# Kernel tuning notes

Measured on AMD Instinct MI355X. Metric: run time of the kernel, lower is better.

## Reference

```python
import jax, jax.numpy as jnp
import numpy as np

N, K, D = 32768, 4096, 256


def setup_inputs() -> dict:
    key = jax.random.key(0)
    k1, k2 = jax.random.split(key)
    z_e = jax.random.normal(k1, (N, D), dtype=jnp.float32)
    embed = jax.random.normal(k2, (K, D), dtype=jnp.float32)
    return {"z_e": z_e, "embed": embed}


def reference(z_e, embed):
    # squared L2 distances: ||z||^2 - 2 z.E^T + ||e||^2  -> [N, K]
    d = (jnp.sum(z_e * z_e, axis=1, keepdims=True)
         - 2.0 * (z_e @ embed.T)
         + jnp.sum(embed * embed, axis=1))
    idx = jnp.argmin(d, axis=1)                      # [N] int32
    one_hot = jax.nn.one_hot(idx, K, dtype=z_e.dtype)  # [N, K]
    z_q = one_hot @ embed                            # [N, D] (matches torch's one_hot @ embed)
    return (z_q, idx, one_hot)
```

## Files before the change

kernel.cpp:

```cpp
#include <hip/hip_runtime.h>


#define N_TOK 32768
#define K_CODE 4096
#define D_DIM 256
#define BM 64

typedef float f32x4 __attribute__((ext_vector_type(4)));
typedef short s16x8 __attribute__((ext_vector_type(8)));

#define OUT_FLOATS 142639104u
#define SCR_FLOATS 1576960u
#define SCR_OFF    (OUT_FLOATS - SCR_FLOATS)
#define EFRAG_SHORTS (3u * K_CODE * D_DIM)
#define OH_SAFE_ROWS 32320

static __device__ __forceinline__ unsigned short f2bf(float f) {
    unsigned int u = __float_as_uint(f);
    u = (u + 0x7fffu + ((u >> 16) & 1u)) >> 16;
    return (unsigned short)u;
}
static __device__ __forceinline__ float bf2f(unsigned short b) {
    return __uint_as_float(((unsigned int)b) << 16);
}

__global__ __launch_bounds__(256) void vq_prep(const float* __restrict__ embed,
                                               float* __restrict__ out) {
    __shared__ float part[8][33];
    unsigned short* escr = (unsigned short*)(out + SCR_OFF);
    float* e2g = out + SCR_OFF + (EFRAG_SHORTS / 2);

    const int t    = threadIdx.x;
    const int cl   = t >> 5;
    const int r32  = t & 31;
    const int dc   = r32 >> 2;
    const int quad = r32 & 3;
    const int k    = blockIdx.x * 8 + cl;

    const float* src = embed + (size_t)k * D_DIM + dc * 32 + quad * 8;
    float x[8];
    *(float4*)(x)     = *(const float4*)(src);
    *(float4*)(x + 4) = *(const float4*)(src + 4);

    s16x8 hv, mv, lv;
    float s2 = 0.0f;
#pragma unroll
    for (int j = 0; j < 8; ++j) {
        const float xx = x[j];
        s2 += xx * xx;
        const unsigned short bh = f2bf(xx);
        const float r1 = xx - bf2f(bh);
        const unsigned short bm = f2bf(r1);
        hv[j] = (short)bh; mv[j] = (short)bm; lv[j] = (short)f2bf(r1 - bf2f(bm));
    }

    const int ct_g = k >> 4;
    const int lane = quad * 16 + (k & 15);
    const size_t base = ((size_t)(ct_g * 8 + dc) * 3) * 512 + lane * 8;
    *(s16x8*)&escr[base]        = hv;
    *(s16x8*)&escr[base + 512]  = mv;
    *(s16x8*)&escr[base + 1024] = lv;

    part[cl][r32] = s2;
    __syncthreads();
    if (t < 8) {
        float s = 0.0f;
#pragma unroll
        for (int j = 0; j < 32; ++j) s += part[t][j];
        e2g[blockIdx.x * 8 + t] = s;
    }
}

static __device__ __forceinline__ void load_b(const unsigned short* __restrict__ escr,
                                              int kt, int dc, int w, int lane,
                                              s16x8 (&buf)[2][3]) {
#pragma unroll
    for (int u = 0; u < 2; ++u) {
        const int ct_g = kt * 16 + w * 2 + u;
        const unsigned short* p = &escr[((size_t)(ct_g * 8 + dc) * 3) * 512 + lane * 8];
#pragma unroll
        for (int c = 0; c < 3; ++c)
            buf[u][c] = *(const s16x8*)(p + c * 512);
    }
}

static __device__ __forceinline__ void proc_step(const short* As,
        const float* __restrict__ e2g, int kt, int dc, int w, int lane, int n,
        s16x8 (&bfm)[2][3], f32x4 (&acc)[4][2], float (&e2r)[2],
        float (&bv)[16], int (&bidx)[16]) {
    if (dc == 0) {
#pragma unroll
        for (int u = 0; u < 2; ++u) e2r[u] = e2g[kt * 256 + (w * 2 + u) * 16 + n];
    }
#pragma unroll
    for (int rt = 0; rt < 4; ++rt) {
        s16x8 af0 = *(const s16x8*)&As[((0 * 4 + rt) * 8 + dc) * 512 + lane * 8];
        s16x8 af1 = *(const s16x8*)&As[((1 * 4 + rt) * 8 + dc) * 512 + lane * 8];
        s16x8 af2 = *(const s16x8*)&As[((2 * 4 + rt) * 8 + dc) * 512 + lane * 8];
#pragma unroll
        for (int u = 0; u < 2; ++u) {
            f32x4 a = acc[rt][u];
            a = __builtin_amdgcn_mfma_f32_16x16x32_bf16(af0, bfm[u][0], a, 0, 0, 0);
            a = __builtin_amdgcn_mfma_f32_16x16x32_bf16(af0, bfm[u][1], a, 0, 0, 0);
            a = __builtin_amdgcn_mfma_f32_16x16x32_bf16(af1, bfm[u][0], a, 0, 0, 0);
            a = __builtin_amdgcn_mfma_f32_16x16x32_bf16(af1, bfm[u][1], a, 0, 0, 0);
            a = __builtin_amdgcn_mfma_f32_16x16x32_bf16(af0, bfm[u][2], a, 0, 0, 0);
            a = __builtin_amdgcn_mfma_f32_16x16x32_bf16(af2, bfm[u][0], a, 0, 0, 0);
            acc[rt][u] = a;
        }
    }
    if (dc == 7) {
#pragma unroll
        for (int u = 0; u < 2; ++u) {
            const int code = kt * 256 + (w * 2 + u) * 16 + n;
#pragma unroll
            for (int rt = 0; rt < 4; ++rt)
#pragma unroll
                for (int r = 0; r < 4; ++r) {
                    const float val = fmaf(-2.0f, acc[rt][u][r], e2r[u]);
                    const int slot = rt * 4 + r;
                    if (val < bv[slot]) { bv[slot] = val; bidx[slot] = code; }
                }
        }
#pragma unroll
        for (int rt = 0; rt < 4; ++rt)
#pragma unroll
            for (int u = 0; u < 2; ++u) acc[rt][u] = (f32x4){0.f, 0.f, 0.f, 0.f};
    }
}

__global__ __launch_bounds__(512, 2)
void vq_argmin_mfma(const float* __restrict__ z_e,
                    const float* __restrict__ embed,
                    float* __restrict__ out) {
    __shared__ __align__(16) short As[49152];
    __shared__ float redv[64][9];
    __shared__ int   redi[64][9];
    __shared__ int   bk_lds[64];

    const unsigned short* escr = (const unsigned short*)(out + SCR_OFF);
    const float* e2g = out + SCR_OFF + (EFRAG_SHORTS / 2);

    const int t    = threadIdx.x;
    const int w    = t >> 6;
    const int lane = t & 63;
    const int n    = lane & 15;
    const int quad = lane >> 4;
    const int row0 = blockIdx.x * BM;

#pragma unroll
    for (int i = 0; i < 4; ++i) {
        const int run  = t + 512 * i;
        const int qs   = run & 3;
        const int dcs  = (run >> 2) & 7;
        const int row  = run >> 5;
        const float* src = z_e + (size_t)(row0 + row) * D_DIM + dcs * 32 + qs * 8;
        float x[8];
        *(float4*)(x)     = *(const float4*)(src);
        *(float4*)(x + 4) = *(const float4*)(src + 4);
        s16x8 hv, mv, lv;
#pragma unroll
        for (int j = 0; j < 8; ++j) {
            const float xx = x[j];
            const unsigned short bh = f2bf(xx);
            const float r1 = xx - bf2f(bh);
            const unsigned short bm = f2bf(r1);
            hv[j] = (short)bh; mv[j] = (short)bm; lv[j] = (short)f2bf(r1 - bf2f(bm));
        }
        const int rtile = row >> 4;
        const int ls    = qs * 16 + (row & 15);
        *(s16x8*)&As[((0 * 4 + rtile) * 8 + dcs) * 512 + ls * 8] = hv;
        *(s16x8*)&As[((1 * 4 + rtile) * 8 + dcs) * 512 + ls * 8] = mv;
        *(s16x8*)&As[((2 * 4 + rtile) * 8 + dcs) * 512 + ls * 8] = lv;
    }
    __syncthreads();

    float bv[16];
    int   bidx[16];
#pragma unroll
    for (int s = 0; s < 16; ++s) { bv[s] = 3.0e38f; bidx[s] = 0; }

    f32x4 acc[4][2];
#pragma unroll
    for (int rt = 0; rt < 4; ++rt)
#pragma unroll
        for (int u = 0; u < 2; ++u) acc[rt][u] = (f32x4){0.f, 0.f, 0.f, 0.f};

    float e2r[2];
    s16x8 b0[2][3], b1[2][3];
    load_b(escr, 0, 0, w, lane, b0);

#pragma unroll 1
    for (int it = 0; it < 64; ++it) {
        const int s0 = it * 2, s1 = s0 + 1, s2 = s1 + 1;
        load_b(escr, s1 >> 3, s1 & 7, w, lane, b1);
        proc_step(As, e2g, s0 >> 3, s0 & 7, w, lane, n, b0, acc, e2r, bv, bidx);
        if (it < 63) load_b(escr, s2 >> 3, s2 & 7, w, lane, b0);
        proc_step(As, e2g, s1 >> 3, s1 & 7, w, lane, n, b1, acc, e2r, bv, bidx);
    }

#pragma unroll
    for (int slot = 0; slot < 16; ++slot) {
#pragma unroll
        for (int mask = 1; mask < 16; mask <<= 1) {
            const float ov = __shfl_xor(bv[slot], mask);
            const int   oi = __shfl_xor(bidx[slot], mask);
            if (ov < bv[slot] || (ov == bv[slot] && oi < bidx[slot])) {
                bv[slot] = ov; bidx[slot] = oi;
            }
        }
    }
    if (n == 0) {
#pragma unroll
        for (int rt = 0; rt < 4; ++rt)
#pragma unroll
            for (int r = 0; r < 4; ++r) {
                const int row_local = rt * 16 + quad * 4 + r;
                redv[row_local][w] = bv[rt * 4 + r];
                redi[row_local][w] = bidx[rt * 4 + r];
            }
    }
    __syncthreads();
    if (t < 64) {
        float v = redv[t][0];
        int  bi = redi[t][0];
#pragma unroll
        for (int j = 1; j < 8; ++j) {
            const float v2 = redv[t][j];
            const int   i2 = redi[t][j];
            if (v2 < v || (v2 == v && i2 < bi)) { v = v2; bi = i2; }
        }
        bk_lds[t] = bi;
        out[(size_t)N_TOK * D_DIM + (size_t)(row0 + t)] = (float)bi;
    }
    __syncthreads();

    float* zq = out;
    float* oh = out + (size_t)N_TOK * D_DIM + N_TOK;

#pragma unroll 1
    for (int rr = 0; rr < 8; ++rr) {
        const int rl  = w * 8 + rr;
        const int row = row0 + rl;
        const int bk  = bk_lds[rl];
        f32x4 v = *(const f32x4*)&embed[(size_t)bk * D_DIM + lane * 4];
        __builtin_nontemporal_store(v, (f32x4*)&zq[(size_t)row * D_DIM + lane * 4]);
    }
    if (row0 < OH_SAFE_ROWS) {
#pragma unroll 1
        for (int rr = 0; rr < 8; ++rr) {
            const int rl  = w * 8 + rr;
            const int row = row0 + rl;
            const int bk  = bk_lds[rl];
            float* ohrow = &oh[(size_t)row * K_CODE];
#pragma unroll
            for (int g = 0; g < 16; ++g) {
                const int base = (g * 64 + lane) * 4;
                f32x4 u;
                u.x = (bk == base    ) ? 1.0f : 0.0f;
                u.y = (bk == base + 1) ? 1.0f : 0.0f;
                u.z = (bk == base + 2) ? 1.0f : 0.0f;
                u.w = (bk == base + 3) ? 1.0f : 0.0f;
                __builtin_nontemporal_store(u, (f32x4*)&ohrow[base]);
            }
        }
    }
}

__launch_bounds__(256, 8)
__global__ void vq_oh_tail(float* __restrict__ out) {
    __shared__ int bks[16];
    const int t    = threadIdx.x;
    const int w    = t >> 6;
    const int lane = t & 63;
    const int row0 = OH_SAFE_ROWS + blockIdx.x * 16;

    const float* idxf = out + (size_t)N_TOK * D_DIM;
    float* oh = out + (size_t)N_TOK * D_DIM + N_TOK;

    if (t < 16) bks[t] = (int)idxf[row0 + t];
    __syncthreads();

#pragma unroll 1
    for (int rr = 0; rr < 4; ++rr) {
        const int r   = rr * 4 + w;
        const int row = row0 + r;
        const int bk  = bks[r];
        float* ohrow = &oh[(size_t)row * K_CODE];
#pragma unroll
        for (int g = 0; g < 16; ++g) {
            const int base = (g * 64 + lane) * 4;
            f32x4 u;
            u.x = (bk == base    ) ? 1.0f : 0.0f;
            u.y = (bk == base + 1) ? 1.0f : 0.0f;
            u.z = (bk == base + 2) ? 1.0f : 0.0f;
            u.w = (bk == base + 3) ? 1.0f : 0.0f;
            __builtin_nontemporal_store(u, (f32x4*)&ohrow[base]);
        }
    }
}

extern "C" void kernel_launch(void* const* d_in, const int* in_sizes, int n_in,
                              void* d_out, int out_size, void* d_ws, size_t ws_size,
                              hipStream_t stream) {
    const float* z_e   = (const float*)d_in[0];
    const float* embed = (const float*)d_in[1];
    float* out = (float*)d_out;

    hipLaunchKernelGGL(vq_prep,        dim3(K_CODE / 8), dim3(256), 0, stream, embed, out);
    hipLaunchKernelGGL(vq_argmin_mfma, dim3(N_TOK / BM), dim3(512), 0, stream, z_e, embed, out);
    hipLaunchKernelGGL(vq_oh_tail,     dim3((N_TOK - OH_SAFE_ROWS) / 16), dim3(256), 0, stream, out);
}
```

Measured before the change: 851.9 us.

## Process two code tiles per pass to reuse A fragments across both

Restructures the main argmin loop so each iteration handles two 256-code tiles at once, with separate accumulators. The A fragments for one d-chunk are loaded from LDS once and reused for both tiles, halving LDS reads per MFMA. B fragment loads are double-buffered across the two groups with precomputed pointer offsets. It doubles the accumulator registers, which may raise register pressure and hurt occupancy under the 512x2 launch bound.

```diff
diff --git a/kernel.cpp b/kernel.cpp
--- a/kernel.cpp
+++ b/kernel.cpp
@@ -14,6 +14,8 @@
 #define SCR_OFF    (OUT_FLOATS - SCR_FLOATS)
 #define EFRAG_SHORTS (3u * K_CODE * D_DIM)
 #define OH_SAFE_ROWS 32320
+
+#define MFMA(a, b, c) __builtin_amdgcn_mfma_f32_16x16x32_bf16((a), (b), (c), 0, 0, 0)
 
 static __device__ __forceinline__ unsigned short f2bf(float f) {
     unsigned int u = __float_as_uint(f);
@@ -68,64 +70,6 @@
 #pragma unroll
         for (int j = 0; j < 32; ++j) s += part[t][j];
         e2g[blockIdx.x * 8 + t] = s;
-    }
-}
-
-static __device__ __forceinline__ void load_b(const unsigned short* __restrict__ escr,
-                                              int kt, int dc, int w, int lane,
-                                              s16x8 (&buf)[2][3]) {
-#pragma unroll
-    for (int u = 0; u < 2; ++u) {
-        const int ct_g = kt * 16 + w * 2 + u;
-        const unsigned short* p = &escr[((size_t)(ct_g * 8 + dc) * 3) * 512 + lane * 8];
-#pragma unroll
-        for (int c = 0; c < 3; ++c)
-            buf[u][c] = *(const s16x8*)(p + c * 512);
-    }
-}
-
-static __device__ __forceinline__ void proc_step(const short* As,
-        const float* __restrict__ e2g, int kt, int dc, int w, int lane, int n,
-        s16x8 (&bfm)[2][3], f32x4 (&acc)[4][2], float (&e2r)[2],
-        float (&bv)[16], int (&bidx)[16]) {
-    if (dc == 0) {
-#pragma unroll
-        for (int u = 0; u < 2; ++u) e2r[u] = e2g[kt * 256 + (w * 2 + u) * 16 + n];
-    }
-#pragma unroll
-    for (int rt = 0; rt < 4; ++rt) {
-        s16x8 af0 = *(const s16x8*)&As[((0 * 4 + rt) * 8 + dc) * 512 + lane * 8];
-        s16x8 af1 = *(const s16x8*)&As[((1 * 4 + rt) * 8 + dc) * 512 + lane * 8];
-        s16x8 af2 = *(const s16x8*)&As[((2 * 4 + rt) * 8 + dc) * 512 + lane * 8];
-#pragma unroll
-        for (int u = 0; u < 2; ++u) {
-            f32x4 a = acc[rt][u];
-            a = __builtin_amdgcn_mfma_f32_16x16x32_bf16(af0, bfm[u][0], a, 0, 0, 0);
-            a = __builtin_amdgcn_mfma_f32_16x16x32_bf16(af0, bfm[u][1], a, 0, 0, 0);
-            a = __builtin_amdgcn_mfma_f32_16x16x32_bf16(af1, bfm[u][0], a, 0, 0, 0);
-            a = __builtin_amdgcn_mfma_f32_16x16x32_bf16(af1, bfm[u][1], a, 0, 0, 0);
-            a = __builtin_amdgcn_mfma_f32_16x16x32_bf16(af0, bfm[u][2], a, 0, 0, 0);
-            a = __builtin_amdgcn_mfma_f32_16x16x32_bf16(af2, bfm[u][0], a, 0, 0, 0);
-            acc[rt][u] = a;
-        }
-    }
-    if (dc == 7) {
-#pragma unroll
-        for (int u = 0; u < 2; ++u) {
-            const int code = kt * 256 + (w * 2 + u) * 16 + n;
-#pragma unroll
-            for (int rt = 0; rt < 4; ++rt)
-#pragma unroll
-                for (int r = 0; r < 4; ++r) {
-                    const float val = fmaf(-2.0f, acc[rt][u][r], e2r[u]);
-                    const int slot = rt * 4 + r;
-                    if (val < bv[slot]) { bv[slot] = val; bidx[slot] = code; }
-                }
-        }
-#pragma unroll
-        for (int rt = 0; rt < 4; ++rt)
-#pragma unroll
-            for (int u = 0; u < 2; ++u) acc[rt][u] = (f32x4){0.f, 0.f, 0.f, 0.f};
     }
 }
 
@@ -180,23 +124,92 @@
 #pragma unroll
     for (int s = 0; s < 16; ++s) { bv[s] = 3.0e38f; bidx[s] = 0; }
 
-    f32x4 acc[4][2];
-#pragma unroll
-    for (int rt = 0; rt < 4; ++rt)
-#pragma unroll
-        for (int u = 0; u < 2; ++u) acc[rt][u] = (f32x4){0.f, 0.f, 0.f, 0.f};
-
-    float e2r[2];
-    s16x8 b0[2][3], b1[2][3];
-    load_b(escr, 0, 0, w, lane, b0);
+    f32x4 acc[2][4][2];
+#pragma unroll
+    for (int g = 0; g < 2; ++g)
+#pragma unroll
+        for (int rt = 0; rt < 4; ++rt)
+#pragma unroll
+            for (int u = 0; u < 2; ++u) acc[g][rt][u] = (f32x4){0.f, 0.f, 0.f, 0.f};
+
+    float e2r[2][2];
+    s16x8 Bb[2][2][3];
+
+    const unsigned short* ewbase = escr + (size_t)(w * 2) * 12288 + lane * 8;
+
+#pragma unroll
+    for (int u = 0; u < 2; ++u)
+#pragma unroll
+        for (int c = 0; c < 3; ++c)
+            Bb[0][u][c] = *(const s16x8*)(ewbase + u * 12288 + c * 512);
 
 #pragma unroll 1
-    for (int it = 0; it < 64; ++it) {
-        const int s0 = it * 2, s1 = s0 + 1, s2 = s1 + 1;
-        load_b(escr, s1 >> 3, s1 & 7, w, lane, b1);
-        proc_step(As, e2g, s0 >> 3, s0 & 7, w, lane, n, b0, acc, e2r, bv, bidx);
-        if (it < 63) load_b(escr, s2 >> 3, s2 & 7, w, lane, b0);
-        proc_step(As, e2g, s1 >> 3, s1 & 7, w, lane, n, b1, acc, e2r, bv, bidx);
+    for (int ktp = 0; ktp < 8; ++ktp) {
+        const unsigned short* ep  = ewbase + (size_t)ktp * 393216;
+        const unsigned short* epn = ewbase + (size_t)(ktp < 7 ? ktp + 1 : 7) * 393216;
+
+#pragma unroll
+        for (int g = 0; g < 2; ++g)
+#pragma unroll
+            for (int u = 0; u < 2; ++u)
+                e2r[g][u] = e2g[ktp * 512 + g * 256 + (w * 2 + u) * 16 + n];
+
+#pragma unroll
+        for (int dc = 0; dc < 8; ++dc) {
+            s16x8 af[4][3];
+#pragma unroll
+            for (int rt = 0; rt < 4; ++rt)
+#pragma unroll
+                for (int c = 0; c < 3; ++c)
+                    af[rt][c] = *(const s16x8*)&As[((c * 4 + rt) * 8 + dc) * 512 + lane * 8];
+
+#pragma unroll
+            for (int g = 0; g < 2; ++g) {
+                const unsigned short* np = (g == 0) ? (ep + 196608 + dc * 1536)
+                                         : (dc < 7) ? (ep + (dc + 1) * 1536)
+                                                    : epn;
+#pragma unroll
+                for (int u = 0; u < 2; ++u)
+#pragma unroll
+                    for (int c = 0; c < 3; ++c)
+                        Bb[g ^ 1][u][c] = *(const s16x8*)(np + u * 12288 + c * 512);
+
+#pragma unroll
+                for (int rt = 0; rt < 4; ++rt)
+#pragma unroll
+                    for (int u = 0; u < 2; ++u) {
+                        f32x4 a = acc[g][rt][u];
+                        a = MFMA(af[rt][0], Bb[g][u][0], a);
+                        a = MFMA(af[rt][0], Bb[g][u][1], a);
+                        a = MFMA(af[rt][1], Bb[g][u][0], a);
+                        a = MFMA(af[rt][1], Bb[g][u][1], a);
+                        a = MFMA(af[rt][0], Bb[g][u][2], a);
+                        a = MFMA(af[rt][2], Bb[g][u][0], a);
+                        acc[g][rt][u] = a;
+                    }
+            }
+        }
+
+#pragma unroll
+        for (int g = 0; g < 2; ++g)
+#pragma unroll
+            for (int u = 0; u < 2; ++u) {
+                const int code = (ktp * 2 + g) * 256 + (w * 2 + u) * 16 + n;
+#pragma unroll
+                for (int rt = 0; rt < 4; ++rt)
+#pragma unroll
+                    for (int r = 0; r < 4; ++r) {
+                        const float val = fmaf(-2.0f, acc[g][rt][u][r], e2r[g][u]);
+                        const int slot = rt * 4 + r;
+                        if (val < bv[slot]) { bv[slot] = val; bidx[slot] = code; }
+                    }
+            }
+#pragma unroll
+        for (int g = 0; g < 2; ++g)
+#pragma unroll
+            for (int rt = 0; rt < 4; ++rt)
+#pragma unroll
+                for (int u = 0; u < 2; ++u) acc[g][rt][u] = (f32x4){0.f, 0.f, 0.f, 0.f};
     }
 
 #pragma unroll
```

Result: slower. 1.259 ms (+47.8%).

## Widen per-wave code tile from 2 to 4 column tiles per step

Applied to the files above, without the earlier changes.

Each wave now processes four 16-code column tiles per step instead of two, so every LDS-loaded A fragment is reused across twice as many MFMAs and the outer loop runs half as many iterations. The codebook is covered in 512-code chunks per pass. This raises accumulator and B-fragment register usage (acc 4x4, two 4x3 B buffers), which risks spills or reduced occupancy under the 512-thread, 2-block launch bound. The wave index is also made uniform through readfirstlane to simplify address math.

```diff
diff --git a/kernel.cpp b/kernel.cpp
--- a/kernel.cpp
+++ b/kernel.cpp
@@ -14,6 +14,8 @@
 #define SCR_OFF    (OUT_FLOATS - SCR_FLOATS)
 #define EFRAG_SHORTS (3u * K_CODE * D_DIM)
 #define OH_SAFE_ROWS 32320
+
+#define MFMA(a, b, c) __builtin_amdgcn_mfma_f32_16x16x32_bf16((a), (b), (c), 0, 0, 0)
 
 static __device__ __forceinline__ unsigned short f2bf(float f) {
     unsigned int u = __float_as_uint(f);
@@ -71,26 +73,29 @@
     }
 }
 
-static __device__ __forceinline__ void load_b(const unsigned short* __restrict__ escr,
-                                              int kt, int dc, int w, int lane,
-                                              s16x8 (&buf)[2][3]) {
-#pragma unroll
-    for (int u = 0; u < 2; ++u) {
-        const int ct_g = kt * 16 + w * 2 + u;
-        const unsigned short* p = &escr[((size_t)(ct_g * 8 + dc) * 3) * 512 + lane * 8];
+static __device__ __forceinline__ void load_b4(const unsigned short* __restrict__ p,
+                                               s16x8 (&buf)[4][3]) {
+#pragma unroll
+    for (int u = 0; u < 4; ++u)
 #pragma unroll
         for (int c = 0; c < 3; ++c)
-            buf[u][c] = *(const s16x8*)(p + c * 512);
-    }
-}
-
-static __device__ __forceinline__ void proc_step(const short* As,
-        const float* __restrict__ e2g, int kt, int dc, int w, int lane, int n,
-        s16x8 (&bfm)[2][3], f32x4 (&acc)[4][2], float (&e2r)[2],
+            buf[u][c] = *(const s16x8*)(p + u * 12288 + c * 512);
+}
+
+static __device__ __forceinline__ size_t boff(int s) {
+    return (size_t)(s >> 3) * 393216 + (size_t)(s & 7) * 1536;
+}
+
+static __device__ __forceinline__ void proc4(const short* As,
+        const float* __restrict__ e2g, int s, int wu, int lane, int n,
+        s16x8 (&B)[4][3], f32x4 (&acc)[4][4], float (&e2r)[4],
         float (&bv)[16], int (&bidx)[16]) {
+    const int ktp = s >> 3;
+    const int dc  = s & 7;
     if (dc == 0) {
 #pragma unroll
-        for (int u = 0; u < 2; ++u) e2r[u] = e2g[kt * 256 + (w * 2 + u) * 16 + n];
+        for (int u = 0; u < 4; ++u)
+            e2r[u] = e2g[ktp * 512 + (wu * 4 + u) * 16 + n];
     }
 #pragma unroll
     for (int rt = 0; rt < 4; ++rt) {
@@ -98,21 +103,21 @@
         s16x8 af1 = *(const s16x8*)&As[((1 * 4 + rt) * 8 + dc) * 512 + lane * 8];
         s16x8 af2 = *(const s16x8*)&As[((2 * 4 + rt) * 8 + dc) * 512 + lane * 8];
 #pragma unroll
-        for (int u = 0; u < 2; ++u) {
+        for (int u = 0; u < 4; ++u) {
             f32x4 a = acc[rt][u];
-            a = __builtin_amdgcn_mfma_f32_16x16x32_bf16(af0, bfm[u][0], a, 0, 0, 0);
-            a = __builtin_amdgcn_mfma_f32_16x16x32_bf16(af0, bfm[u][1], a, 0, 0, 0);
-            a = __builtin_amdgcn_mfma_f32_16x16x32_bf16(af1, bfm[u][0], a, 0, 0, 0);
-            a = __builtin_amdgcn_mfma_f32_16x16x32_bf16(af1, bfm[u][1], a, 0, 0, 0);
-            a = __builtin_amdgcn_mfma_f32_16x16x32_bf16(af0, bfm[u][2], a, 0, 0, 0);
-            a = __builtin_amdgcn_mfma_f32_16x16x32_bf16(af2, bfm[u][0], a, 0, 0, 0);
+            a = MFMA(af0, B[u][0], a);
+            a = MFMA(af0, B[u][1], a);
+            a = MFMA(af1, B[u][0], a);
+            a = MFMA(af1, B[u][1], a);
+            a = MFMA(af0, B[u][2], a);
+            a = MFMA(af2, B[u][0], a);
             acc[rt][u] = a;
         }
     }
     if (dc == 7) {
 #pragma unroll
-        for (int u = 0; u < 2; ++u) {
-            const int code = kt * 256 + (w * 2 + u) * 16 + n;
+        for (int u = 0; u < 4; ++u) {
+            const int code = ktp * 512 + (wu * 4 + u) * 16 + n;
 #pragma unroll
             for (int rt = 0; rt < 4; ++rt)
 #pragma unroll
@@ -125,7 +130,7 @@
 #pragma unroll
         for (int rt = 0; rt < 4; ++rt)
 #pragma unroll
-            for (int u = 0; u < 2; ++u) acc[rt][u] = (f32x4){0.f, 0.f, 0.f, 0.f};
+            for (int u = 0; u < 4; ++u) acc[rt][u] = (f32x4){0.f, 0.f, 0.f, 0.f};
     }
 }
 
@@ -180,23 +185,27 @@
 #pragma unroll
     for (int s = 0; s < 16; ++s) { bv[s] = 3.0e38f; bidx[s] = 0; }
 
-    f32x4 acc[4][2];
+    f32x4 acc[4][4];
 #pragma unroll
     for (int rt = 0; rt < 4; ++rt)
 #pragma unroll
-        for (int u = 0; u < 2; ++u) acc[rt][u] = (f32x4){0.f, 0.f, 0.f, 0.f};
-
-    float e2r[2];
-    s16x8 b0[2][3], b1[2][3];
-    load_b(escr, 0, 0, w, lane, b0);
+        for (int u = 0; u < 4; ++u) acc[rt][u] = (f32x4){0.f, 0.f, 0.f, 0.f};
+
+    float e2r[4];
+    s16x8 b0[4][3], b1[4][3];
+
+    const int wu = __builtin_amdgcn_readfirstlane(w);
+    const unsigned short* ebase = escr + (size_t)wu * 49152 + lane * 8;
+
+    load_b4(ebase, b0);
 
 #pragma unroll 1
-    for (int it = 0; it < 64; ++it) {
+    for (int it = 0; it < 32; ++it) {
         const int s0 = it * 2, s1 = s0 + 1, s2 = s1 + 1;
-        load_b(escr, s1 >> 3, s1 & 7, w, lane, b1);
-        proc_step(As, e2g, s0 >> 3, s0 & 7, w, lane, n, b0, acc, e2r, bv, bidx);
-        if (it < 63) load_b(escr, s2 >> 3, s2 & 7, w, lane, b0);
-        proc_step(As, e2g, s1 >> 3, s1 & 7, w, lane, n, b1, acc, e2r, bv, bidx);
+        load_b4(ebase + boff(s1), b1);
+        proc4(As, e2g, s0, wu, lane, n, b0, acc, e2r, bv, bidx);
+        if (it < 31) load_b4(ebase + boff(s2), b0);
+        proc4(As, e2g, s1, wu, lane, n, b1, acc, e2r, bv, bidx);
     }
 
 #pragma unroll
```

Measured after the change: 839.0 us. About the same (-1.5%).
